# Optimization experiments

Measured on AMD Instinct MI355X. Metric: run time of the kernel, lower is better.

Reference implementation:

```python
import jax, jax.numpy as jnp
import numpy as np

B, S, HID = 2, 2048, 1024
NH, HD = 16, 64  # op_heads, head_size; op_size = NH*HD = 1024


def setup_inputs() -> dict:
    key = jax.random.key(0)
    k1, k2, k3 = jax.random.split(key, 3)
    hidden_states = jax.random.normal(k1, (B, S, HID), dtype=jnp.float32)
    # Linear weights stored as [in, out] for x @ W + b
    Wqk = jax.random.normal(k2, (HID, 2 * NH * HD), dtype=jnp.float32) * (HID ** -0.5)
    bqk = jnp.zeros((2 * NH * HD,), dtype=jnp.float32)
    Wv = jax.random.normal(k3, (HID, NH * HD), dtype=jnp.float32) * (HID ** -0.5)
    bv = jnp.zeros((NH * HD,), dtype=jnp.float32)
    return {"hidden_states": hidden_states, "Wqk": Wqk, "bqk": bqk, "Wv": Wv, "bv": bv}


def _split_heads(t):
    # [B, S, NH*HD] -> [B, NH, S, HD]
    b, s, _ = t.shape
    return t.reshape(b, s, NH, HD).transpose(0, 2, 1, 3)


def reference(hidden_states, Wqk, bqk, Wv, bv):
    op_size = NH * HD
    qk = hidden_states @ Wqk + bqk                      # [B, S, 2*op_size]
    query, key = qk[..., :op_size], qk[..., op_size:]
    value = hidden_states @ Wv + bv                     # [B, S, op_size]
    q = _split_heads(query)                             # [B, H, S, D]
    k = _split_heads(key)
    v = _split_heads(value)
    # scores: [B, H, Sq, Sk], scaled by sqrt(head_dim) (scale_attn_weights=True)
    scores = jnp.einsum('bhqd,bhkd->bhqk', q, k) / jnp.asarray(HD ** 0.5, q.dtype)
    s = scores.shape[-1]
    causal = jnp.tril(jnp.ones((s, s), dtype=bool))     # [S, S]
    mask_value = jnp.finfo(scores.dtype).min
    scores = jnp.where(causal, scores, mask_value)
    attn = jax.nn.softmax(scores, axis=-1)              # dropout is identity (eval)
    out = jnp.einsum('bhqk,bhkd->bhqd', attn, v)        # [B, H, S, D]
    out = out.transpose(0, 2, 1, 3).reshape(out.shape[0], out.shape[2], NH * HD)
    return out
```

## Files before the change

kernel.cpp:

```cpp
#include <hip/hip_runtime.h>

typedef float floatx4 __attribute__((ext_vector_type(4)));
typedef float floatx16 __attribute__((ext_vector_type(16)));
typedef __bf16 bf16x8 __attribute__((ext_vector_type(8)));
typedef unsigned short u16x8 __attribute__((ext_vector_type(8)));
typedef unsigned short u16x4 __attribute__((ext_vector_type(4)));

__device__ __forceinline__ unsigned short f2bf(float f) {
    unsigned u = __float_as_uint(f);
    u += 0x7fffu + ((u >> 16) & 1u);
    return (unsigned short)(u >> 16);
}

#if __has_builtin(__builtin_amdgcn_cvt_pk_bf16_f32)
__device__ __forceinline__ unsigned pk2(float a, float b) {
    typedef __bf16 bf16x2 __attribute__((ext_vector_type(2)));
    union { bf16x2 v; unsigned u; } cv;
    cv.v = __builtin_amdgcn_cvt_pk_bf16_f32(a, b);
    return cv.u;
}
#else
__device__ __forceinline__ unsigned pk2(float a, float b) {
    return (unsigned)f2bf(a) | ((unsigned)f2bf(b) << 16);
}
#endif

#if __has_builtin(__builtin_amdgcn_exp2f)
__device__ __forceinline__ float fast_exp2(float x) { return __builtin_amdgcn_exp2f(x); }
#else
__device__ __forceinline__ float fast_exp2(float x) { return __exp2f(x); }
#endif

__global__ __launch_bounds__(256) void k_prep(const float* __restrict__ hidden,
                                              const float* __restrict__ Wqk,
                                              const float* __restrict__ Wv,
                                              unsigned short* __restrict__ Af,
                                              unsigned short* __restrict__ Wtf) {
    __shared__ unsigned short t[64][68];
    const int tid = threadIdx.x;
    const int lane = tid & 63;
    const int w = tid >> 6;
    const int l15 = lane & 15;
    const int quad = lane >> 4;
    if (blockIdx.x < 512) {
        const int mt = blockIdx.x >> 1;
        const int half = blockIdx.x & 1;
        const int m0 = mt * 16;
#pragma unroll
        for (int r = 0; r < 4; ++r) {
            const int kc = half * 16 + r * 4 + w;
            const float* src = hidden + (size_t)(m0 + l15) * 1024 + kc * 32 + quad * 8;
            float4 a = *(const float4*)src;
            float4 b = *(const float4*)(src + 4);
            u16x8 o;
            o[0] = f2bf(a.x); o[1] = f2bf(a.y); o[2] = f2bf(a.z); o[3] = f2bf(a.w);
            o[4] = f2bf(b.x); o[5] = f2bf(b.y); o[6] = f2bf(b.z); o[7] = f2bf(b.w);
            *(u16x8*)(Af + ((size_t)(mt * 32 + kc) * 64 + lane) * 8) = o;
        }
        return;
    }
    const int bx = blockIdx.x - 512;
    const int n0 = (bx % 48) * 64;
    const int k0 = (bx / 48) * 64;
    const int nl = tid & 63;
    const int kb = tid >> 6;
    const int ng = n0 + nl;
#pragma unroll
    for (int i = 0; i < 16; ++i) {
        int kl = kb + i * 4;
        float v = (n0 < 2048) ? Wqk[(size_t)(k0 + kl) * 2048 + ng]
                              : Wv[(size_t)(k0 + kl) * 1024 + (ng - 2048)];
        t[nl][kl] = f2bf(v);
    }
    __syncthreads();
#pragma unroll
    for (int pi = 0; pi < 2; ++pi) {
        const int p = tid + pi * 256;
        const int ntl = p >> 7;
        const int kcl = (p >> 6) & 1;
        const int lo = p & 63;
        const int nloc = ntl * 16 + (lo & 15);
        const int kloc = kcl * 32 + (lo >> 4) * 8;
        u16x8 o;
#pragma unroll
        for (int j = 0; j < 8; ++j) o[j] = t[nloc][kloc + j];
        const int nt_g = (n0 >> 4) + ntl;
        const int kc_g = (k0 >> 5) + kcl;
        *(u16x8*)(Wtf + ((size_t)(nt_g * 32 + kc_g) * 64 + lo) * 8) = o;
    }
}

__global__ __launch_bounds__(256, 3) void k_gemm_qkv(
    const unsigned short* __restrict__ Af,
    const unsigned short* __restrict__ Wtf,
    const float* __restrict__ bqk, const float* __restrict__ bvv,
    unsigned short* __restrict__ Qf, unsigned short* __restrict__ Kf,
    unsigned short* __restrict__ Vf) {
    const int tid = threadIdx.x;
    const int lane = tid & 63;
    const int w = tid >> 6;
    const int l15 = lane & 15;
    const int quad = lane >> 4;
    const int gb = blockIdx.x;
    const int q = gb >> 3;
    const int m0 = ((((gb & 7) << 2) | (q & 3))) * 128;
    const int n0 = (q >> 2) * 128;
    const bool isV = (n0 >= 2048);
    const int wm = (w & 1) * 64;
    const int wn = (w >> 1) * 64;

    const unsigned short* Ab = Af  + ((size_t)((m0 >> 4) + (w & 1) * 4) * 32) * 512 + lane * 8;
    const unsigned short* Bb = Wtf + ((size_t)((n0 >> 4) + (w >> 1) * 4) * 32) * 512 + lane * 8;

    floatx4 acc[4][4] = {};
    bf16x8 af[4], bfr[4];
#pragma unroll
    for (int i = 0; i < 4; ++i) {
        af[i]  = *(const bf16x8*)(Ab + (size_t)(i * 32) * 512);
        bfr[i] = *(const bf16x8*)(Bb + (size_t)(i * 32) * 512);
    }

    for (int kc = 0; kc < 32; ++kc) {
        bf16x8 an[4], bn[4];
        if (kc < 31) {
#pragma unroll
            for (int i = 0; i < 4; ++i) {
                an[i] = *(const bf16x8*)(Ab + (size_t)(i * 32 + kc + 1) * 512);
                bn[i] = *(const bf16x8*)(Bb + (size_t)(i * 32 + kc + 1) * 512);
            }
        }
        if (!isV) {
#pragma unroll
            for (int mi = 0; mi < 4; ++mi)
#pragma unroll
                for (int ni = 0; ni < 4; ++ni)
                    acc[mi][ni] = __builtin_amdgcn_mfma_f32_16x16x32_bf16(bfr[ni], af[mi],
                                                                          acc[mi][ni], 0, 0, 0);
        } else {
#pragma unroll
            for (int mi = 0; mi < 4; ++mi)
#pragma unroll
                for (int ni = 0; ni < 4; ++ni)
                    acc[mi][ni] = __builtin_amdgcn_mfma_f32_16x16x32_bf16(af[mi], bfr[ni],
                                                                          acc[mi][ni], 0, 0, 0);
        }
#pragma unroll
        for (int i = 0; i < 4; ++i) { af[i] = an[i]; bfr[i] = bn[i]; }
    }

    if (!isV) {
        const bool isQ = (n0 < 1024);
        unsigned short* dst = isQ ? Qf : Kf;
        const float scale = isQ ? 0.18033688011112042f : 1.0f;
#pragma unroll
        for (int mi = 0; mi < 4; ++mi) {
            const int m = m0 + wm + mi * 16 + l15;
            const int b = m >> 11, s = m & 2047;
            const int t = s >> 5, cc = s & 31;
#pragma unroll
            for (int ni = 0; ni < 4; ++ni) {
                const int nb = n0 + wn + ni * 16 + (quad << 2);
                const float4 bq = *(const float4*)(bqk + nb);
                const int hd = isQ ? nb : nb - 1024;
                const int h = hd >> 6, d = hd & 63;
                const int kb = d >> 4, hhd = (d >> 3) & 1, jj = d & 7;
                const int bh = b * 16 + h;
                u16x4 o4;
                o4[0] = f2bf((acc[mi][ni][0] + bq.x) * scale);
                o4[1] = f2bf((acc[mi][ni][1] + bq.y) * scale);
                o4[2] = f2bf((acc[mi][ni][2] + bq.z) * scale);
                o4[3] = f2bf((acc[mi][ni][3] + bq.w) * scale);
                size_t idx = ((((size_t)(bh * 64 + t) * 4 + kb) * 2 + hhd) * 32 + cc) * 8 + jj;
                *(u16x4*)(dst + idx) = o4;
            }
        }
    } else {
#pragma unroll
        for (int ni = 0; ni < 4; ++ni) {
            const int n = n0 + wn + ni * 16 + l15;
            const float bias = bvv[n - 2048];
            const int hd = n - 2048;
            const int h = hd >> 6, d = hd & 63;
            const int dt = d >> 5, cc = d & 31;
#pragma unroll
            for (int mi = 0; mi < 4; ++mi) {
                const int m = m0 + wm + mi * 16 + (quad << 2);
                const int b = m >> 11, s = m & 2047;
                const int bh = b * 16 + h, t = s >> 5, kvr = s & 31;
                const int mb = kvr >> 4, hhv = (kvr >> 3) & 1, jj0 = s & 7;
                u16x4 o4;
#pragma unroll
                for (int r = 0; r < 4; ++r) o4[r] = f2bf(acc[mi][ni][r] + bias);
                size_t idx = (((((size_t)(bh * 64 + t) * 2 + mb) * 2 + dt) * 2 + hhv) * 32 + cc) * 8 + jj0;
                *(u16x4*)(Vf + idx) = o4;
            }
        }
    }
}

__global__ __launch_bounds__(256, 3) void k_attn(
    const unsigned short* __restrict__ Qf, const unsigned short* __restrict__ Kf,
    const unsigned short* __restrict__ Vf, float* __restrict__ out,
    float* __restrict__ Op1, float* __restrict__ l0, float* __restrict__ l1) {
    const int tid = threadIdx.x;
    const int lane = tid & 63;
    const int w = tid >> 6;
    const int c = lane & 31;
    const int hh = lane >> 5;
    const int gb = blockIdx.x;
    const int xcd = gb & 7;
    const int idx = gb >> 3;
    const int bh = xcd + ((idx & 3) << 3);
    const int u = idx >> 2;
    int a, mode;
    if (u < 8) { a = 8 + u; mode = 1; }
    else {
        const int i = u - 8;
        if ((i & 1) == 0) { a = 7 - (i >> 1); mode = 0; }
        else              { a = 15 - (i >> 1); mode = 2; }
    }
    const int j = 4 * a + w;
    const int t0 = (mode == 2) ? 32 : 0;
    const int t1 = (mode == 1) ? 31 : j;
    const int q_abs = j * 32 + c;

    bf16x8 qf[4];
    {
        const unsigned short* qp = Qf + (size_t)(bh * 64 + j) * 2048 + lane * 8;
#pragma unroll
        for (int kb = 0; kb < 4; ++kb) qf[kb] = *(const bf16x8*)(qp + kb * 512);
    }
    const unsigned short* kbase = Kf + (size_t)bh * (64 * 2048) + lane * 8;
    const unsigned short* vbase = Vf + (size_t)bh * (64 * 2048) + lane * 8;

    floatx16 o2[2] = {};
    float ls0 = 0.f, ls1 = 0.f;

    bf16x8 kf[4];
    {
        const unsigned short* kp = kbase + (size_t)t0 * 2048;
#pragma unroll
        for (int kb = 0; kb < 4; ++kb) kf[kb] = *(const bf16x8*)(kp + kb * 512);
    }

    for (int t = t0; t <= t1; ++t) {
        const unsigned short* vp = vbase + (size_t)t * 2048;
        bf16x8 vf[4];
#pragma unroll
        for (int f = 0; f < 4; ++f) vf[f] = *(const bf16x8*)(vp + f * 512);

        floatx16 st = {};
#pragma unroll
        for (int kb = 0; kb < 4; ++kb)
            st = __builtin_amdgcn_mfma_f32_32x32x16_bf16(kf[kb], qf[kb], st, 0, 0, 0);

        bf16x8 kn[4];
        if (t < t1) {
            const unsigned short* kpn = kbase + (size_t)(t + 1) * 2048;
#pragma unroll
            for (int kb = 0; kb < 4; ++kb) kn[kb] = *(const bf16x8*)(kpn + kb * 512);
        }

        if (t == j) {
#pragma unroll
            for (int i = 0; i < 16; ++i) {
                const int kvr = (i & 3) + 8 * (i >> 2) + 4 * hh;
                if (kvr > c) st[i] = -1e30f;
            }
        }

        float a0 = 0.f, a1 = 0.f, a2 = 0.f, a3 = 0.f;
#pragma unroll
        for (int i = 0; i < 16; i += 4) {
            float p0 = fast_exp2(st[i + 0]);
            float p1 = fast_exp2(st[i + 1]);
            float p2 = fast_exp2(st[i + 2]);
            float p3 = fast_exp2(st[i + 3]);
            st[i + 0] = p0; st[i + 1] = p1; st[i + 2] = p2; st[i + 3] = p3;
            a0 += p0; a1 += p1; a2 += p2; a3 += p3;
        }
        ls0 += a0 + a2; ls1 += a1 + a3;

#pragma unroll
        for (int mb = 0; mb < 2; ++mb) {
            const int rb = mb * 8;
            unsigned p0 = pk2(st[rb + 0], st[rb + 1]);
            unsigned p1 = pk2(st[rb + 2], st[rb + 3]);
            unsigned p2 = pk2(st[rb + 4], st[rb + 5]);
            unsigned p3 = pk2(st[rb + 6], st[rb + 7]);
            unsigned sA = hh ? p0 : p2;
            unsigned sB = hh ? p1 : p3;
            unsigned rA = (unsigned)__shfl_xor((int)sA, 32, 64);
            unsigned rB = (unsigned)__shfl_xor((int)sB, 32, 64);
            union { unsigned u4[4]; bf16x8 v; } pf;
            if (hh == 0) { pf.u4[0] = p0; pf.u4[1] = p1; pf.u4[2] = rA; pf.u4[3] = rB; }
            else         { pf.u4[0] = rA; pf.u4[1] = rB; pf.u4[2] = p2; pf.u4[3] = p3; }
#pragma unroll
            for (int dt = 0; dt < 2; ++dt)
                o2[dt] = __builtin_amdgcn_mfma_f32_32x32x16_bf16(vf[mb * 2 + dt], pf.v,
                                                                 o2[dt], 0, 0, 0);
        }
#pragma unroll
        for (int kb = 0; kb < 4; ++kb) kf[kb] = kn[kb];
    }

    const int b = bh >> 4, head = bh & 15;
    float lrow = ls0 + ls1;
    lrow += __shfl_xor(lrow, 32, 64);
    if (mode == 0) {
        const float inv = 1.0f / lrow;
        float* op = out + (size_t)(b * 2048 + q_abs) * 1024 + head * 64;
#pragma unroll
        for (int dt = 0; dt < 2; ++dt)
#pragma unroll
            for (int rr = 0; rr < 4; ++rr) {
                float4 v4 = make_float4(o2[dt][rr * 4 + 0] * inv, o2[dt][rr * 4 + 1] * inv,
                                        o2[dt][rr * 4 + 2] * inv, o2[dt][rr * 4 + 3] * inv);
                *(float4*)(op + dt * 32 + rr * 8 + hh * 4) = v4;
            }
    } else {
        const int qr = q_abs - 1024;
        float* op;
        if (mode == 1) {
            if (hh == 0) l0[bh * 1024 + qr] = lrow;
            op = out + (size_t)(b * 2048 + q_abs) * 1024 + head * 64;
        } else {
            if (hh == 0) l1[bh * 1024 + qr] = lrow;
            op = Op1 + (size_t)(bh * 1024 + qr) * 64;
        }
#pragma unroll
        for (int dt = 0; dt < 2; ++dt)
#pragma unroll
            for (int rr = 0; rr < 4; ++rr) {
                float4 v4 = make_float4(o2[dt][rr * 4 + 0], o2[dt][rr * 4 + 1],
                                        o2[dt][rr * 4 + 2], o2[dt][rr * 4 + 3]);
                *(float4*)(op + dt * 32 + rr * 8 + hh * 4) = v4;
            }
    }
}

__global__ __launch_bounds__(256) void k_comb(const float* __restrict__ Op1,
                                              const float* __restrict__ l0,
                                              const float* __restrict__ l1,
                                              float* __restrict__ out) {
    const int idx = blockIdx.x * 256 + threadIdx.x;
    const int bh = idx >> 14;
    const int rem = idx & 16383;
    const int qr = rem >> 4;
    const int d4 = (rem & 15) << 2;
    const float inv = 1.0f / (l0[bh * 1024 + qr] + l1[bh * 1024 + qr]);
    const int b = bh >> 4, h = bh & 15;
    float* op = out + (size_t)(b * 2048 + 1024 + qr) * 1024 + h * 64 + d4;
    const float* pp = Op1 + (size_t)(bh * 1024 + qr) * 64 + d4;
    float4 a = *(const float4*)op;
    float4 p = *(const float4*)pp;
    float4 r = make_float4((a.x + p.x) * inv, (a.y + p.y) * inv,
                           (a.z + p.z) * inv, (a.w + p.w) * inv);
    *(float4*)op = r;
}

extern "C" void kernel_launch(void* const* d_in, const int* in_sizes, int n_in,
                              void* d_out, int out_size, void* d_ws, size_t ws_size,
                              hipStream_t stream) {
    const float* hidden = (const float*)d_in[0];
    const float* Wqk    = (const float*)d_in[1];
    const float* bqk    = (const float*)d_in[2];
    const float* Wv     = (const float*)d_in[3];
    const float* bvv    = (const float*)d_in[4];
    float* out = (float*)d_out;

    unsigned short* Af  = (unsigned short*)d_ws;
    unsigned short* Wtf = Af + 4096 * 1024;
    unsigned short* Qf  = Wtf + 3072 * 1024;
    unsigned short* Kf  = Qf + 32 * 2048 * 64;
    unsigned short* Vf  = Kf + 32 * 2048 * 64;
    float* Op1 = (float*)d_ws;
    float* l0  = Op1 + 32 * 1024 * 64;
    float* l1  = l0 + 32 * 1024;

    k_prep<<<1280, 256, 0, stream>>>(hidden, Wqk, Wv, Af, Wtf);
    k_gemm_qkv<<<768, 256, 0, stream>>>(Af, Wtf, bqk, bvv, Qf, Kf, Vf);
    k_attn<<<768, 256, 0, stream>>>(Qf, Kf, Vf, out, Op1, l0, l1);
    k_comb<<<2048, 256, 0, stream>>>(Op1, l0, l1, out);
}
```

Measured before the change: 151.0 us.

## Stage QKV GEMM tiles through LDS with direct global-to-LDS loads

The QKV projection GEMM used to have each wave read its A and B fragments straight from global memory into registers, with register double-buffering. Now the block cooperatively copies two k-chunks of the A and B tiles into shared memory using global_load_lds, and each wave reads its fragments from LDS. This stops the two waves that need the same tile from fetching it twice from global memory. In exchange it adds two block barriers per step and removes the prefetch overlap, so loads are no longer hidden behind the MFMAs.

```diff
diff --git a/kernel.cpp b/kernel.cpp
--- a/kernel.cpp
+++ b/kernel.cpp
@@ -5,6 +5,10 @@
 typedef __bf16 bf16x8 __attribute__((ext_vector_type(8)));
 typedef unsigned short u16x8 __attribute__((ext_vector_type(8)));
 typedef unsigned short u16x4 __attribute__((ext_vector_type(4)));
+
+#define GLDS16(g, l) __builtin_amdgcn_global_load_lds( \
+    (__attribute__((address_space(1))) void*)(g), \
+    (__attribute__((address_space(3))) void*)(l), 16, 0, 0)
 
 __device__ __forceinline__ unsigned short f2bf(float f) {
     unsigned u = __float_as_uint(f);
@@ -96,6 +100,8 @@
     const float* __restrict__ bqk, const float* __restrict__ bvv,
     unsigned short* __restrict__ Qf, unsigned short* __restrict__ Kf,
     unsigned short* __restrict__ Vf) {
+    __shared__ unsigned short As[16 * 512];
+    __shared__ unsigned short Bs[16 * 512];
     const int tid = threadIdx.x;
     const int lane = tid & 63;
     const int w = tid >> 6;
@@ -106,46 +112,53 @@
     const int m0 = ((((gb & 7) << 2) | (q & 3))) * 128;
     const int n0 = (q >> 2) * 128;
     const bool isV = (n0 >= 2048);
-    const int wm = (w & 1) * 64;
-    const int wn = (w >> 1) * 64;
-
-    const unsigned short* Ab = Af  + ((size_t)((m0 >> 4) + (w & 1) * 4) * 32) * 512 + lane * 8;
-    const unsigned short* Bb = Wtf + ((size_t)((n0 >> 4) + (w >> 1) * 4) * 32) * 512 + lane * 8;
+    const int wmt = (w & 1) * 4;
+    const int wnt = (w >> 1) * 4;
+    const int wm = wmt * 16;
+    const int wn = wnt * 16;
 
     floatx4 acc[4][4] = {};
-    bf16x8 af[4], bfr[4];
-#pragma unroll
-    for (int i = 0; i < 4; ++i) {
-        af[i]  = *(const bf16x8*)(Ab + (size_t)(i * 32) * 512);
-        bfr[i] = *(const bf16x8*)(Bb + (size_t)(i * 32) * 512);
-    }
-
-    for (int kc = 0; kc < 32; ++kc) {
-        bf16x8 an[4], bn[4];
-        if (kc < 31) {
-#pragma unroll
-            for (int i = 0; i < 4; ++i) {
-                an[i] = *(const bf16x8*)(Ab + (size_t)(i * 32 + kc + 1) * 512);
-                bn[i] = *(const bf16x8*)(Bb + (size_t)(i * 32 + kc + 1) * 512);
-            }
-        }
-        if (!isV) {
+
+    const unsigned short* AgW = Af  + ((size_t)((m0 >> 4) + w * 2) * 32) * 512 + lane * 8;
+    const unsigned short* BgW = Wtf + ((size_t)((n0 >> 4) + w * 2) * 32) * 512 + lane * 8;
+    unsigned short* AsW = As + (w * 4) * 512;
+    unsigned short* BsW = Bs + (w * 4) * 512;
+
+    for (int kc = 0; kc < 32; kc += 2) {
+        __syncthreads();
+#pragma unroll
+        for (int mi = 0; mi < 2; ++mi)
+#pragma unroll
+            for (int p = 0; p < 2; ++p) {
+                GLDS16(AgW + (size_t)(mi * 32 + kc + p) * 512, AsW + (mi * 2 + p) * 512);
+                GLDS16(BgW + (size_t)(mi * 32 + kc + p) * 512, BsW + (mi * 2 + p) * 512);
+            }
+        __syncthreads();
+#pragma unroll
+        for (int h = 0; h < 2; ++h) {
+            bf16x8 af[4], bfr[4];
 #pragma unroll
             for (int mi = 0; mi < 4; ++mi)
-#pragma unroll
-                for (int ni = 0; ni < 4; ++ni)
-                    acc[mi][ni] = __builtin_amdgcn_mfma_f32_16x16x32_bf16(bfr[ni], af[mi],
-                                                                          acc[mi][ni], 0, 0, 0);
-        } else {
-#pragma unroll
-            for (int mi = 0; mi < 4; ++mi)
-#pragma unroll
-                for (int ni = 0; ni < 4; ++ni)
-                    acc[mi][ni] = __builtin_amdgcn_mfma_f32_16x16x32_bf16(af[mi], bfr[ni],
-                                                                          acc[mi][ni], 0, 0, 0);
-        }
-#pragma unroll
-        for (int i = 0; i < 4; ++i) { af[i] = an[i]; bfr[i] = bn[i]; }
+                af[mi] = *(const bf16x8*)(As + ((wmt + mi) * 2 + h) * 512 + lane * 8);
+#pragma unroll
+            for (int ni = 0; ni < 4; ++ni)
+                bfr[ni] = *(const bf16x8*)(Bs + ((wnt + ni) * 2 + h) * 512 + lane * 8);
+            if (!isV) {
+#pragma unroll
+                for (int mi = 0; mi < 4; ++mi)
+#pragma unroll
+                    for (int ni = 0; ni < 4; ++ni)
+                        acc[mi][ni] = __builtin_amdgcn_mfma_f32_16x16x32_bf16(bfr[ni], af[mi],
+                                                                              acc[mi][ni], 0, 0, 0);
+            } else {
+#pragma unroll
+                for (int mi = 0; mi < 4; ++mi)
+#pragma unroll
+                    for (int ni = 0; ni < 4; ++ni)
+                        acc[mi][ni] = __builtin_amdgcn_mfma_f32_16x16x32_bf16(af[mi], bfr[ni],
+                                                                              acc[mi][ni], 0, 0, 0);
+            }
+        }
     }
 
     if (!isV) {
```

Result: slower. 166.8 us (+10.5%).

## Process two query tiles per wave in attention to reuse K/V fragments

Applied to the files above, without the earlier changes.

Each wave now handles two adjacent 32-row query tiles and shares every loaded K and V fragment between both. Blocks shrink from four waves to two, so the grid still covers the same query range. This halves the K/V global loads per query row. In exchange it roughly doubles accumulator and score registers, lowers occupancy, and adds some wasted masked work on the diagonal tile for the first query tile.

```diff
diff --git a/kernel.cpp b/kernel.cpp
--- a/kernel.cpp
+++ b/kernel.cpp
@@ -198,7 +198,7 @@
     }
 }
 
-__global__ __launch_bounds__(256, 3) void k_attn(
+__global__ __launch_bounds__(128, 2) void k_attn(
     const unsigned short* __restrict__ Qf, const unsigned short* __restrict__ Kf,
     const unsigned short* __restrict__ Vf, float* __restrict__ out,
     float* __restrict__ Op1, float* __restrict__ l0, float* __restrict__ l1) {
@@ -219,22 +219,27 @@
         if ((i & 1) == 0) { a = 7 - (i >> 1); mode = 0; }
         else              { a = 15 - (i >> 1); mode = 2; }
     }
-    const int j = 4 * a + w;
+    const int jA = 4 * a + 2 * w;
+    const int jB = jA + 1;
     const int t0 = (mode == 2) ? 32 : 0;
-    const int t1 = (mode == 1) ? 31 : j;
-    const int q_abs = j * 32 + c;
-
-    bf16x8 qf[4];
+    const int t1 = (mode == 1) ? 31 : jB;
+    const int qA = jA * 32 + c;
+    const int qB = jB * 32 + c;
+
+    bf16x8 qfA[4], qfB[4];
     {
-        const unsigned short* qp = Qf + (size_t)(bh * 64 + j) * 2048 + lane * 8;
-#pragma unroll
-        for (int kb = 0; kb < 4; ++kb) qf[kb] = *(const bf16x8*)(qp + kb * 512);
+        const unsigned short* qp = Qf + (size_t)(bh * 64 + jA) * 2048 + lane * 8;
+#pragma unroll
+        for (int kb = 0; kb < 4; ++kb) {
+            qfA[kb] = *(const bf16x8*)(qp + kb * 512);
+            qfB[kb] = *(const bf16x8*)(qp + 2048 + kb * 512);
+        }
     }
     const unsigned short* kbase = Kf + (size_t)bh * (64 * 2048) + lane * 8;
     const unsigned short* vbase = Vf + (size_t)bh * (64 * 2048) + lane * 8;
 
-    floatx16 o2[2] = {};
-    float ls0 = 0.f, ls1 = 0.f;
+    floatx16 oA[2] = {}, oB[2] = {};
+    float lsA = 0.f, lsB = 0.f;
 
     bf16x8 kf[4];
     {
@@ -249,10 +254,12 @@
 #pragma unroll
         for (int f = 0; f < 4; ++f) vf[f] = *(const bf16x8*)(vp + f * 512);
 
-        floatx16 st = {};
-#pragma unroll
-        for (int kb = 0; kb < 4; ++kb)
-            st = __builtin_amdgcn_mfma_f32_32x32x16_bf16(kf[kb], qf[kb], st, 0, 0, 0);
+        floatx16 stA = {}, stB = {};
+#pragma unroll
+        for (int kb = 0; kb < 4; ++kb) {
+            stA = __builtin_amdgcn_mfma_f32_32x32x16_bf16(kf[kb], qfA[kb], stA, 0, 0, 0);
+            stB = __builtin_amdgcn_mfma_f32_32x32x16_bf16(kf[kb], qfB[kb], stB, 0, 0, 0);
+        }
 
         bf16x8 kn[4];
         if (t < t1) {
@@ -261,81 +268,100 @@
             for (int kb = 0; kb < 4; ++kb) kn[kb] = *(const bf16x8*)(kpn + kb * 512);
         }
 
-        if (t == j) {
+        if (t >= jA) {
+            const int kv0 = t * 32;
 #pragma unroll
             for (int i = 0; i < 16; ++i) {
-                const int kvr = (i & 3) + 8 * (i >> 2) + 4 * hh;
-                if (kvr > c) st[i] = -1e30f;
-            }
-        }
-
-        float a0 = 0.f, a1 = 0.f, a2 = 0.f, a3 = 0.f;
-#pragma unroll
-        for (int i = 0; i < 16; i += 4) {
-            float p0 = fast_exp2(st[i + 0]);
-            float p1 = fast_exp2(st[i + 1]);
-            float p2 = fast_exp2(st[i + 2]);
-            float p3 = fast_exp2(st[i + 3]);
-            st[i + 0] = p0; st[i + 1] = p1; st[i + 2] = p2; st[i + 3] = p3;
-            a0 += p0; a1 += p1; a2 += p2; a3 += p3;
-        }
-        ls0 += a0 + a2; ls1 += a1 + a3;
+                const int kva = kv0 + (i & 3) + 8 * (i >> 2) + 4 * hh;
+                if (kva > qA) stA[i] = -1e30f;
+                if (kva > qB) stB[i] = -1e30f;
+            }
+        }
+
+        float aa = 0.f, ab = 0.f;
+#pragma unroll
+        for (int i = 0; i < 16; ++i) {
+            float pA = fast_exp2(stA[i]);
+            float pB = fast_exp2(stB[i]);
+            stA[i] = pA; stB[i] = pB;
+            aa += pA; ab += pB;
+        }
+        lsA += aa; lsB += ab;
 
 #pragma unroll
         for (int mb = 0; mb < 2; ++mb) {
             const int rb = mb * 8;
-            unsigned p0 = pk2(st[rb + 0], st[rb + 1]);
-            unsigned p1 = pk2(st[rb + 2], st[rb + 3]);
-            unsigned p2 = pk2(st[rb + 4], st[rb + 5]);
-            unsigned p3 = pk2(st[rb + 6], st[rb + 7]);
-            unsigned sA = hh ? p0 : p2;
-            unsigned sB = hh ? p1 : p3;
-            unsigned rA = (unsigned)__shfl_xor((int)sA, 32, 64);
-            unsigned rB = (unsigned)__shfl_xor((int)sB, 32, 64);
-            union { unsigned u4[4]; bf16x8 v; } pf;
-            if (hh == 0) { pf.u4[0] = p0; pf.u4[1] = p1; pf.u4[2] = rA; pf.u4[3] = rB; }
-            else         { pf.u4[0] = rA; pf.u4[1] = rB; pf.u4[2] = p2; pf.u4[3] = p3; }
+            unsigned pA0 = pk2(stA[rb + 0], stA[rb + 1]);
+            unsigned pA1 = pk2(stA[rb + 2], stA[rb + 3]);
+            unsigned pA2 = pk2(stA[rb + 4], stA[rb + 5]);
+            unsigned pA3 = pk2(stA[rb + 6], stA[rb + 7]);
+            unsigned pB0 = pk2(stB[rb + 0], stB[rb + 1]);
+            unsigned pB1 = pk2(stB[rb + 2], stB[rb + 3]);
+            unsigned pB2 = pk2(stB[rb + 4], stB[rb + 5]);
+            unsigned pB3 = pk2(stB[rb + 6], stB[rb + 7]);
+            unsigned sA0 = hh ? pA0 : pA2, sA1 = hh ? pA1 : pA3;
+            unsigned sB0 = hh ? pB0 : pB2, sB1 = hh ? pB1 : pB3;
+            unsigned rA0 = (unsigned)__shfl_xor((int)sA0, 32, 64);
+            unsigned rA1 = (unsigned)__shfl_xor((int)sA1, 32, 64);
+            unsigned rB0 = (unsigned)__shfl_xor((int)sB0, 32, 64);
+            unsigned rB1 = (unsigned)__shfl_xor((int)sB1, 32, 64);
+            union { unsigned u4[4]; bf16x8 v; } pfA, pfB;
+            if (hh == 0) {
+                pfA.u4[0] = pA0; pfA.u4[1] = pA1; pfA.u4[2] = rA0; pfA.u4[3] = rA1;
+                pfB.u4[0] = pB0; pfB.u4[1] = pB1; pfB.u4[2] = rB0; pfB.u4[3] = rB1;
+            } else {
+                pfA.u4[0] = rA0; pfA.u4[1] = rA1; pfA.u4[2] = pA2; pfA.u4[3] = pA3;
+                pfB.u4[0] = rB0; pfB.u4[1] = rB1; pfB.u4[2] = pB2; pfB.u4[3] = pB3;
+            }
+#pragma unroll
+            for (int dt = 0; dt < 2; ++dt) {
+                oA[dt] = __builtin_amdgcn_mfma_f32_32x32x16_bf16(vf[mb * 2 + dt], pfA.v,
+                                                                 oA[dt], 0, 0, 0);
+                oB[dt] = __builtin_amdgcn_mfma_f32_32x32x16_bf16(vf[mb * 2 + dt], pfB.v,
+                                                                 oB[dt], 0, 0, 0);
+            }
+        }
+#pragma unroll
+        for (int kb = 0; kb < 4; ++kb) kf[kb] = kn[kb];
+    }
+
+    const int b = bh >> 4, head = bh & 15;
+#pragma unroll
+    for (int tile = 0; tile < 2; ++tile) {
+        const int q_abs = tile ? qB : qA;
+        floatx16* o2 = tile ? oB : oA;
+        float lrow = tile ? lsB : lsA;
+        lrow += __shfl_xor(lrow, 32, 64);
+        if (mode == 0) {
+            const float inv = 1.0f / lrow;
+            float* op = out + (size_t)(b * 2048 + q_abs) * 1024 + head * 64;
 #pragma unroll
             for (int dt = 0; dt < 2; ++dt)
-                o2[dt] = __builtin_amdgcn_mfma_f32_32x32x16_bf16(vf[mb * 2 + dt], pf.v,
-                                                                 o2[dt], 0, 0, 0);
-        }
-#pragma unroll
-        for (int kb = 0; kb < 4; ++kb) kf[kb] = kn[kb];
-    }
-
-    const int b = bh >> 4, head = bh & 15;
-    float lrow = ls0 + ls1;
-    lrow += __shfl_xor(lrow, 32, 64);
-    if (mode == 0) {
-        const float inv = 1.0f / lrow;
-        float* op = out + (size_t)(b * 2048 + q_abs) * 1024 + head * 64;
-#pragma unroll
-        for (int dt = 0; dt < 2; ++dt)
-#pragma unroll
-            for (int rr = 0; rr < 4; ++rr) {
-                float4 v4 = make_float4(o2[dt][rr * 4 + 0] * inv, o2[dt][rr * 4 + 1] * inv,
-                                        o2[dt][rr * 4 + 2] * inv, o2[dt][rr * 4 + 3] * inv);
-                *(float4*)(op + dt * 32 + rr * 8 + hh * 4) = v4;
-            }
-    } else {
-        const int qr = q_abs - 1024;
-        float* op;
-        if (mode == 1) {
-            if (hh == 0) l0[bh * 1024 + qr] = lrow;
-            op = out + (size_t)(b * 2048 + q_abs) * 1024 + head * 64;
+#pragma unroll
+                for (int rr = 0; rr < 4; ++rr) {
+                    float4 v4 = make_float4(o2[dt][rr * 4 + 0] * inv, o2[dt][rr * 4 + 1] * inv,
+                                            o2[dt][rr * 4 + 2] * inv, o2[dt][rr * 4 + 3] * inv);
+                    *(float4*)(op + dt * 32 + rr * 8 + hh * 4) = v4;
+                }
         } else {
-            if (hh == 0) l1[bh * 1024 + qr] = lrow;
-            op = Op1 + (size_t)(bh * 1024 + qr) * 64;
-        }
-#pragma unroll
-        for (int dt = 0; dt < 2; ++dt)
-#pragma unroll
-            for (int rr = 0; rr < 4; ++rr) {
-                float4 v4 = make_float4(o2[dt][rr * 4 + 0], o2[dt][rr * 4 + 1],
-                                        o2[dt][rr * 4 + 2], o2[dt][rr * 4 + 3]);
-                *(float4*)(op + dt * 32 + rr * 8 + hh * 4) = v4;
-            }
+            const int qr = q_abs - 1024;
+            float* op;
+            if (mode == 1) {
+                if (hh == 0) l0[bh * 1024 + qr] = lrow;
+                op = out + (size_t)(b * 2048 + q_abs) * 1024 + head * 64;
+            } else {
+                if (hh == 0) l1[bh * 1024 + qr] = lrow;
+                op = Op1 + (size_t)(bh * 1024 + qr) * 64;
+            }
+#pragma unroll
+            for (int dt = 0; dt < 2; ++dt)
+#pragma unroll
+                for (int rr = 0; rr < 4; ++rr) {
+                    float4 v4 = make_float4(o2[dt][rr * 4 + 0], o2[dt][rr * 4 + 1],
+                                            o2[dt][rr * 4 + 2], o2[dt][rr * 4 + 3]);
+                    *(float4*)(op + dt * 32 + rr * 8 + hh * 4) = v4;
+                }
+        }
     }
 }
 
@@ -380,6 +406,6 @@
 
     k_prep<<<1280, 256, 0, stream>>>(hidden, Wqk, Wv, Af, Wtf);
     k_gemm_qkv<<<768, 256, 0, stream>>>(Af, Wtf, bqk, bvv, Qf, Kf, Vf);
-    k_attn<<<768, 256, 0, stream>>>(Qf, Kf, Vf, out, Op1, l0, l1);
+    k_attn<<<768, 128, 0, stream>>>(Qf, Kf, Vf, out, Op1, l0, l1);
     k_comb<<<2048, 256, 0, stream>>>(Op1, l0, l1, out);
 }
```

Result: slower. 162.8 us (+7.8%).
